# Performance work log

Hardware: AMD Instinct MI355X
Metric: run time of the kernel (lower is better)

The kernel has to match this reference:

```python
import jax, jax.numpy as jnp
import numpy as np

N_NODES = 100000
N_EDGES = 1600000
D_FEAT = 64
K = 5


def setup_inputs() -> dict:
    key = jax.random.key(0)
    k1, k2, k3 = jax.random.split(key, 3)
    feat = jax.random.normal(k1, (N_NODES, D_FEAT), dtype=jnp.float32)
    theta = jnp.asarray([1.0, -0.8, 0.45, -0.2, 0.08], dtype=jnp.float32)
    src = jax.random.randint(k2, (N_EDGES,), 0, N_NODES, dtype=jnp.int32)
    dst = jax.random.randint(k3, (N_EDGES,), 0, N_NODES, dtype=jnp.int32)
    return {"feat": feat, "theta": theta, "src": src, "dst": dst}


def reference(feat, theta, src, dst):
    n = feat.shape[0]
    # in-degrees: number of edges terminating at each node, clamped to >= 1
    deg = jax.ops.segment_sum(jnp.ones_like(dst, dtype=feat.dtype), dst, num_segments=n)
    d_invsqrt = jnp.maximum(deg, 1.0) ** -0.5  # [N]
    d_invsqrt = d_invsqrt[:, None]  # [N, 1]

    def unn_laplacian(x):
        scaled = x * d_invsqrt  # [N, D]
        agg = jax.ops.segment_sum(scaled[src], dst, num_segments=n)  # [N, D]
        return x - agg * d_invsqrt

    h = theta[0] * feat
    for k in range(1, theta.shape[0]):
        feat = unn_laplacian(feat)
        h = h + theta[k] * feat
    return h
```

## Files before the change

### kernel.cpp

```cpp
#include <hip/hip_runtime.h>
#include <hip/hip_bf16.h>
#include <hip/hip_fp16.h>

#define WG 256
#define WGB 1024
#define D 64
#define MAXNB 1024

__device__ inline float ld_mixed(const void* p, int bf, long i) {
    if (bf) {
        unsigned short u = ((const unsigned short*)p)[i];
        return __uint_as_float(((unsigned int)u) << 16);
    }
    return ((const float*)p)[i];
}

__global__ void k_detect(const void* __restrict__ theta, int* __restrict__ flag) {
    unsigned int w = *(const unsigned int*)theta;
    *flag = (w == 0x3F800000u) ? 0 : 1;
}


__global__ __launch_bounds__(WGB) void kc_hist(
        const int* __restrict__ dst, int E, int NBc, int CPB,
        int* __restrict__ histmat) {
    __shared__ int h[MAXNB];
    int B = blockIdx.x, t = threadIdx.x;
    for (int i = t; i < NBc; i += WGB) h[i] = 0;
    __syncthreads();
    int base = B * CPB;
    int end = min(base + CPB, E);
    for (int e = base + t; e < end; e += WGB)
        atomicAdd(&h[dst[e] >> 8], 1);
    __syncthreads();
    for (int i = t; i < NBc; i += WGB)
        histmat[(long)i * NBc + B] = h[i];
}

__global__ void k_scan1(const int* __restrict__ in, int M,
                        int* __restrict__ out, int* __restrict__ part) {
    __shared__ int s[WG];
    int g = blockIdx.x * WG + threadIdx.x;
    int t = threadIdx.x;
    s[t] = (g < M) ? in[g] : 0;
    __syncthreads();
    for (int o = 1; o < WG; o <<= 1) {
        int v = (t >= o) ? s[t - o] : 0;
        __syncthreads();
        s[t] += v;
        __syncthreads();
    }
    if (g < M) out[g + 1] = s[t];
    if (t == WG - 1) part[blockIdx.x] = s[t];
}

__global__ void k_scan2(int* __restrict__ part, int P) {
    __shared__ int s[1024];
    int t = threadIdx.x;
    s[t] = (t < P) ? part[t] : 0;
    __syncthreads();
    for (int o = 1; o < 1024; o <<= 1) {
        int v = (t >= o) ? s[t - o] : 0;
        __syncthreads();
        s[t] += v;
        __syncthreads();
    }
    if (t < P) part[t] = (t == 0) ? 0 : s[t - 1];
}

__global__ void k_scan3(int* __restrict__ out, int M, const int* __restrict__ part) {
    int g = blockIdx.x * WG + threadIdx.x;
    if (g < M) out[g + 1] += part[blockIdx.x];
    if (g == 0) out[0] = 0;
}

__global__ __launch_bounds__(WGB) void kc_scatter(
        const int* __restrict__ src, const int* __restrict__ dst, int E,
        int NBc, int CPB, const int* __restrict__ scanned,
        int2* __restrict__ tmp) {
    __shared__ int off[MAXNB];
    int B = blockIdx.x, t = threadIdx.x;
    for (int i = t; i < NBc; i += WGB)
        off[i] = scanned[(long)i * NBc + B];
    __syncthreads();
    int base = B * CPB;
    int end = min(base + CPB, E);
    for (int e = base + t; e < end; e += WGB) {
        int d = dst[e];
        int pos = atomicAdd(&off[d >> 8], 1);
        int2 p; p.x = src[e]; p.y = d;
        tmp[pos] = p;
    }
}

__global__ __launch_bounds__(WGB) void kf(
        const int2* __restrict__ tmp, const int* __restrict__ scanned,
        int NBc, int N, int E, int* __restrict__ ptr,
        float* __restrict__ dinv, float* __restrict__ dsqrt,
        int* __restrict__ csr) {
    __shared__ int h[256];
    __shared__ int pfx[256];
    __shared__ int cnt[256];
    int B = blockIdx.x, t = threadIdx.x;
    int rbase = scanned[(long)B * NBc];
    int rend  = scanned[(long)(B + 1) * NBc];
    if (t < 256) h[t] = 0;
    __syncthreads();
    for (int e = rbase + t; e < rend; e += WGB)
        atomicAdd(&h[tmp[e].y & 255], 1);
    __syncthreads();
    if (t < 256) pfx[t] = h[t];
    __syncthreads();
    for (int o = 1; o < 256; o <<= 1) {
        int v = 0;
        if (t < 256 && t >= o) v = pfx[t - o];
        __syncthreads();
        if (t < 256) pfx[t] += v;
        __syncthreads();
    }
    if (t < 256) {
        int ex = pfx[t] - h[t];
        int node = B * 256 + t;
        if (node < N) {
            ptr[node] = rbase + ex;
            float d = (float)h[t];
            d = d < 1.f ? 1.f : d;
            dinv[node]  = rsqrtf(d);
            dsqrt[node] = sqrtf(d);
        }
        cnt[t] = rbase + ex;
    }
    if (B == 0 && t == 0) ptr[N] = E;
    __syncthreads();
    for (int e = rbase + t; e < rend; e += WGB) {
        int2 p = tmp[e];
        int pos = atomicAdd(&cnt[p.y & 255], 1);
        csr[pos] = p.x;
    }
}


__global__ void k_init(const void* __restrict__ feat, const void* __restrict__ theta,
                       const int* __restrict__ flag, const float* __restrict__ dinv,
                       long NF, __half* __restrict__ xs, __half* __restrict__ h) {
    int bf = *flag;
    long g = (long)blockIdx.x * WG + threadIdx.x;
    if (g < NF) {
        float f = ld_mixed(feat, bf, g);
        float th0 = ld_mixed(theta, bf, 0);
        float w = dinv[g >> 6];
        xs[g] = __float2half_rn(f * w);
        h[g]  = __float2half_rn(th0 * f);
    }
}

__global__ __launch_bounds__(WG) void k_spmv(
        const __half* __restrict__ xs,
        const float* __restrict__ dinv, const float* __restrict__ dsqrt,
        const int* __restrict__ ptr, const int* __restrict__ csr,
        const void* __restrict__ theta, const int* __restrict__ flag, int k,
        int N, __half* __restrict__ xsn, __half* __restrict__ h,
        void* __restrict__ out, int last) {
    int wv = (int)(((unsigned)blockIdx.x * blockDim.x + threadIdx.x) >> 6);
    int lane = threadIdx.x & 63;
    int node = 2 * wv + (lane >> 5);
    int l = lane & 31;
    bool valid = node < N;
    int nc = valid ? node : 0;
    int s0 = ptr[nc];
    int s1 = valid ? ptr[nc + 1] : s0;

    const __half2* xs2 = (const __half2*)xs;
    float ax = 0.f, ay = 0.f;
    int e = s0;
    for (; e + 8 <= s1; e += 8) {
        int idx[8];
#pragma unroll
        for (int j = 0; j < 8; ++j) idx[j] = csr[e + j];
        __half2 a[8];
#pragma unroll
        for (int j = 0; j < 8; ++j) a[j] = xs2[idx[j] * 32 + l];
#pragma unroll
        for (int j = 0; j < 8; ++j) {
            float2 f = __half22float2(a[j]);
            ax += f.x; ay += f.y;
        }
    }
    if (e + 4 <= s1) {
        int idx[4];
#pragma unroll
        for (int j = 0; j < 4; ++j) idx[j] = csr[e + j];
        __half2 a[4];
#pragma unroll
        for (int j = 0; j < 4; ++j) a[j] = xs2[idx[j] * 32 + l];
#pragma unroll
        for (int j = 0; j < 4; ++j) {
            float2 f = __half22float2(a[j]);
            ax += f.x; ay += f.y;
        }
        e += 4;
    }
    for (; e < s1; ++e) {
        float2 f = __half22float2(xs2[csr[e] * 32 + l]);
        ax += f.x; ay += f.y;
    }

    if (!valid) return;
    long o = (long)node * 32 + l;
    float w = dinv[node];
    float ds = dsqrt[node];
    float2 xsv = __half22float2(xs2[o]);
    float vx = xsv.x * ds - w * ax;
    float vy = xsv.y * ds - w * ay;
    int bf = *flag;
    float th = ld_mixed(theta, bf, k);
    float2 hv = __half22float2(((const __half2*)h)[o]);
    hv.x += th * vx;
    hv.y += th * vy;
    if (last) {
        if (bf) {
            __hip_bfloat162 r;
            r.x = __float2bfloat16(hv.x);
            r.y = __float2bfloat16(hv.y);
            ((__hip_bfloat162*)out)[o] = r;
        } else {
            float2 r; r.x = hv.x; r.y = hv.y;
            ((float2*)out)[o] = r;
        }
    } else {
        ((__half2*)xsn)[o] = __floats2half2_rn(vx * w, vy * w);
        ((__half2*)h)[o]   = __floats2half2_rn(hv.x, hv.y);
    }
}

extern "C" void kernel_launch(void* const* d_in, const int* in_sizes, int n_in,
                              void* d_out, int out_size, void* d_ws, size_t ws_size,
                              hipStream_t stream) {
    const void* feat  = d_in[0];
    const void* theta = d_in[1];
    const int*  src   = (const int*)d_in[2];
    const int*  dst   = (const int*)d_in[3];
    long NF = in_sizes[0];
    int  N  = (int)(NF / D);
    int  E  = in_sizes[2];

    int NBc = (N + 255) >> 8;
    int CPB = (E + NBc - 1) / NBc;
    int M   = NBc * NBc;

    char* w = (char*)d_ws;
    size_t off = 0;
    auto alloc = [&](size_t b) -> void* {
        void* p = w + off;
        off = (off + b + 255) & ~(size_t)255;
        return p;
    };
    int*    histmat = (int*)alloc((size_t)M * 4);
    int*    scanned = (int*)alloc(((size_t)M + 1) * 4);
    int*    part    = (int*)alloc(1024 * 4);
    int2*   tmp     = (int2*)alloc((size_t)E * 8);
    int*    ptr     = (int*)alloc(((size_t)N + 1) * 4);
    int*    csr     = (int*)alloc((size_t)E * 4);
    float*  dinv    = (float*)alloc((size_t)N * 4);
    float*  dsqrt   = (float*)alloc((size_t)N * 4);
    int*    flag    = (int*)alloc(4);
    __half* xs_a    = (__half*)alloc((size_t)NF * 2);
    __half* xs_b    = (__half*)alloc((size_t)NF * 2);
    __half* h       = (__half*)alloc((size_t)NF * 2);

    int sbl = (M + WG - 1) / WG;
    int fbl = (int)((NF + WG - 1) / WG);
    int wbl = ((N + 1) / 2 + 3) / 4;

    k_detect<<<1, 1, 0, stream>>>(theta, flag);
    kc_hist<<<NBc, WGB, 0, stream>>>(dst, E, NBc, CPB, histmat);
    k_scan1<<<sbl, WG, 0, stream>>>(histmat, M, scanned, part);
    k_scan2<<<1, 1024, 0, stream>>>(part, sbl);
    k_scan3<<<sbl, WG, 0, stream>>>(scanned, M, part);
    kc_scatter<<<NBc, WGB, 0, stream>>>(src, dst, E, NBc, CPB, scanned, tmp);
    kf<<<NBc, WGB, 0, stream>>>(tmp, scanned, NBc, N, E, ptr, dinv, dsqrt, csr);
    k_init<<<fbl, WG, 0, stream>>>(feat, theta, flag, dinv, NF, xs_a, h);

    __half* xa = xs_a;
    __half* xb = xs_b;
    for (int k = 1; k <= 4; ++k) {
        int last = (k == 4);
        k_spmv<<<wbl, WG, 0, stream>>>(xa, dinv, dsqrt, ptr, csr, theta, flag, k,
                                       N, xb, h, d_out, last);
        __half* t = xa; xa = xb; xb = t;
    }
}
```

Measured before the change: 297.0 us.

## Fold detect and scan stages into neighbors, pack CSR temp, add nontemporal accesses

Removes the detect, scan2 and scan3 launches by moving flag detection into the histogram kernel and recomputing the block-partial scan redundantly inside the scatter and finalize kernels. The temporary edge buffer is packed from int2 to a single 32-bit word, with src in the low 24 bits and the local dst in the high 8 bits, halving its traffic. Nontemporal loads and stores are added for csr indices and the h/xs streams in init and spmv. The 24-bit src packing assumes fewer than 16M nodes, and every scatter/finalize block now does a redundant 1024-wide scan.

```diff
diff --git a/kernel.cpp b/kernel.cpp
--- a/kernel.cpp
+++ b/kernel.cpp
@@ -15,17 +15,17 @@
     return ((const float*)p)[i];
 }
 
-__global__ void k_detect(const void* __restrict__ theta, int* __restrict__ flag) {
-    unsigned int w = *(const unsigned int*)theta;
-    *flag = (w == 0x3F800000u) ? 0 : 1;
-}
-
 
 __global__ __launch_bounds__(WGB) void kc_hist(
         const int* __restrict__ dst, int E, int NBc, int CPB,
-        int* __restrict__ histmat) {
+        int* __restrict__ histmat,
+        const void* __restrict__ theta, int* __restrict__ flag) {
     __shared__ int h[MAXNB];
     int B = blockIdx.x, t = threadIdx.x;
+    if (B == 0 && t == 0) {
+        unsigned int w = *(const unsigned int*)theta;
+        *flag = (w == 0x3F800000u) ? 0 : 1;
+    }
     for (int i = t; i < NBc; i += WGB) h[i] = 0;
     __syncthreads();
     int base = B * CPB;
@@ -42,7 +42,8 @@
     __shared__ int s[WG];
     int g = blockIdx.x * WG + threadIdx.x;
     int t = threadIdx.x;
-    s[t] = (g < M) ? in[g] : 0;
+    int v0 = (g < M) ? in[g] : 0;
+    s[t] = v0;
     __syncthreads();
     for (int o = 1; o < WG; o <<= 1) {
         int v = (t >= o) ? s[t - o] : 0;
@@ -50,64 +51,79 @@
         s[t] += v;
         __syncthreads();
     }
-    if (g < M) out[g + 1] = s[t];
+    if (g < M) out[g] = s[t] - v0;
     if (t == WG - 1) part[blockIdx.x] = s[t];
-}
-
-__global__ void k_scan2(int* __restrict__ part, int P) {
-    __shared__ int s[1024];
-    int t = threadIdx.x;
-    s[t] = (t < P) ? part[t] : 0;
-    __syncthreads();
-    for (int o = 1; o < 1024; o <<= 1) {
-        int v = (t >= o) ? s[t - o] : 0;
-        __syncthreads();
-        s[t] += v;
-        __syncthreads();
-    }
-    if (t < P) part[t] = (t == 0) ? 0 : s[t - 1];
-}
-
-__global__ void k_scan3(int* __restrict__ out, int M, const int* __restrict__ part) {
-    int g = blockIdx.x * WG + threadIdx.x;
-    if (g < M) out[g + 1] += part[blockIdx.x];
-    if (g == 0) out[0] = 0;
 }
 
 __global__ __launch_bounds__(WGB) void kc_scatter(
         const int* __restrict__ src, const int* __restrict__ dst, int E,
-        int NBc, int CPB, const int* __restrict__ scanned,
-        int2* __restrict__ tmp) {
+        int NBc, int CPB, const int* __restrict__ outx,
+        const int* __restrict__ part, int P,
+        unsigned int* __restrict__ tmp) {
     __shared__ int off[MAXNB];
+    __shared__ int ps[1024];
+    __shared__ int pex[1024];
     int B = blockIdx.x, t = threadIdx.x;
-    for (int i = t; i < NBc; i += WGB)
-        off[i] = scanned[(long)i * NBc + B];
+    int pv = (t < P) ? part[t] : 0;
+    ps[t] = pv;
+    __syncthreads();
+    for (int o = 1; o < 1024; o <<= 1) {
+        int v = (t >= o) ? ps[t - o] : 0;
+        __syncthreads();
+        ps[t] += v;
+        __syncthreads();
+    }
+    pex[t] = ps[t] - pv;
+    __syncthreads();
+    for (int i = t; i < NBc; i += WGB) {
+        long g = (long)i * NBc + B;
+        off[i] = outx[g] + pex[g >> 8];
+    }
     __syncthreads();
     int base = B * CPB;
     int end = min(base + CPB, E);
     for (int e = base + t; e < end; e += WGB) {
         int d = dst[e];
         int pos = atomicAdd(&off[d >> 8], 1);
-        int2 p; p.x = src[e]; p.y = d;
-        tmp[pos] = p;
+        tmp[pos] = (unsigned)src[e] | ((unsigned)(d & 255) << 24);
     }
 }
 
 __global__ __launch_bounds__(WGB) void kf(
-        const int2* __restrict__ tmp, const int* __restrict__ scanned,
+        const unsigned int* __restrict__ tmp, const int* __restrict__ outx,
+        const int* __restrict__ part, int P,
         int NBc, int N, int E, int* __restrict__ ptr,
         float* __restrict__ dinv, float* __restrict__ dsqrt,
         int* __restrict__ csr) {
     __shared__ int h[256];
     __shared__ int pfx[256];
     __shared__ int cnt[256];
+    __shared__ int ps[1024];
+    __shared__ int pex[1024];
     int B = blockIdx.x, t = threadIdx.x;
-    int rbase = scanned[(long)B * NBc];
-    int rend  = scanned[(long)(B + 1) * NBc];
+    int pv = (t < P) ? part[t] : 0;
+    ps[t] = pv;
+    __syncthreads();
+    for (int o = 1; o < 1024; o <<= 1) {
+        int v = (t >= o) ? ps[t - o] : 0;
+        __syncthreads();
+        ps[t] += v;
+        __syncthreads();
+    }
+    pex[t] = ps[t] - pv;
+    __syncthreads();
+    long g1 = (long)B * NBc;
+    int rbase = outx[g1] + pex[g1 >> 8];
+    int rend;
+    if (B == NBc - 1) rend = E;
+    else {
+        long g2 = (long)(B + 1) * NBc;
+        rend = outx[g2] + pex[g2 >> 8];
+    }
     if (t < 256) h[t] = 0;
     __syncthreads();
     for (int e = rbase + t; e < rend; e += WGB)
-        atomicAdd(&h[tmp[e].y & 255], 1);
+        atomicAdd(&h[tmp[e] >> 24], 1);
     __syncthreads();
     if (t < 256) pfx[t] = h[t];
     __syncthreads();
@@ -133,9 +149,9 @@
     if (B == 0 && t == 0) ptr[N] = E;
     __syncthreads();
     for (int e = rbase + t; e < rend; e += WGB) {
-        int2 p = tmp[e];
-        int pos = atomicAdd(&cnt[p.y & 255], 1);
-        csr[pos] = p.x;
+        unsigned p = tmp[e];
+        int pos = atomicAdd(&cnt[p >> 24], 1);
+        csr[pos] = (int)(p & 0xFFFFFF);
     }
 }
 
@@ -150,7 +166,9 @@
         float th0 = ld_mixed(theta, bf, 0);
         float w = dinv[g >> 6];
         xs[g] = __float2half_rn(f * w);
-        h[g]  = __float2half_rn(th0 * f);
+        __half hv = __float2half_rn(th0 * f);
+        unsigned short hr = *(unsigned short*)&hv;
+        __builtin_nontemporal_store(hr, (unsigned short*)h + g);
     }
 }
 
@@ -176,7 +194,7 @@
     for (; e + 8 <= s1; e += 8) {
         int idx[8];
 #pragma unroll
-        for (int j = 0; j < 8; ++j) idx[j] = csr[e + j];
+        for (int j = 0; j < 8; ++j) idx[j] = __builtin_nontemporal_load(&csr[e + j]);
         __half2 a[8];
 #pragma unroll
         for (int j = 0; j < 8; ++j) a[j] = xs2[idx[j] * 32 + l];
@@ -189,7 +207,7 @@
     if (e + 4 <= s1) {
         int idx[4];
 #pragma unroll
-        for (int j = 0; j < 4; ++j) idx[j] = csr[e + j];
+        for (int j = 0; j < 4; ++j) idx[j] = __builtin_nontemporal_load(&csr[e + j]);
         __half2 a[4];
 #pragma unroll
         for (int j = 0; j < 4; ++j) a[j] = xs2[idx[j] * 32 + l];
@@ -214,7 +232,8 @@
     float vy = xsv.y * ds - w * ay;
     int bf = *flag;
     float th = ld_mixed(theta, bf, k);
-    float2 hv = __half22float2(((const __half2*)h)[o]);
+    unsigned hraw = __builtin_nontemporal_load((const unsigned int*)h + o);
+    float2 hv = __half22float2(*(__half2*)&hraw);
     hv.x += th * vx;
     hv.y += th * vy;
     if (last) {
@@ -228,8 +247,10 @@
             ((float2*)out)[o] = r;
         }
     } else {
-        ((__half2*)xsn)[o] = __floats2half2_rn(vx * w, vy * w);
-        ((__half2*)h)[o]   = __floats2half2_rn(hv.x, hv.y);
+        __half2 xw = __floats2half2_rn(vx * w, vy * w);
+        __builtin_nontemporal_store(*(unsigned*)&xw, (unsigned int*)xsn + o);
+        __half2 hw = __floats2half2_rn(hv.x, hv.y);
+        __builtin_nontemporal_store(*(unsigned*)&hw, (unsigned int*)h + o);
     }
 }
 
@@ -247,6 +268,7 @@
     int NBc = (N + 255) >> 8;
     int CPB = (E + NBc - 1) / NBc;
     int M   = NBc * NBc;
+    int sbl = (M + WG - 1) / WG;
 
     char* w = (char*)d_ws;
     size_t off = 0;
@@ -255,30 +277,26 @@
         off = (off + b + 255) & ~(size_t)255;
         return p;
     };
-    int*    histmat = (int*)alloc((size_t)M * 4);
-    int*    scanned = (int*)alloc(((size_t)M + 1) * 4);
-    int*    part    = (int*)alloc(1024 * 4);
-    int2*   tmp     = (int2*)alloc((size_t)E * 8);
-    int*    ptr     = (int*)alloc(((size_t)N + 1) * 4);
-    int*    csr     = (int*)alloc((size_t)E * 4);
-    float*  dinv    = (float*)alloc((size_t)N * 4);
-    float*  dsqrt   = (float*)alloc((size_t)N * 4);
-    int*    flag    = (int*)alloc(4);
-    __half* xs_a    = (__half*)alloc((size_t)NF * 2);
-    __half* xs_b    = (__half*)alloc((size_t)NF * 2);
-    __half* h       = (__half*)alloc((size_t)NF * 2);
-
-    int sbl = (M + WG - 1) / WG;
+    int*      histmat = (int*)alloc((size_t)M * 4);
+    int*      outx    = (int*)alloc((size_t)M * 4);
+    int*      part    = (int*)alloc(1024 * 4);
+    unsigned* tmp     = (unsigned*)alloc((size_t)E * 4);
+    int*      ptr     = (int*)alloc(((size_t)N + 1) * 4);
+    int*      csr     = (int*)alloc((size_t)E * 4);
+    float*    dinv    = (float*)alloc((size_t)N * 4);
+    float*    dsqrt   = (float*)alloc((size_t)N * 4);
+    int*      flag    = (int*)alloc(4);
+    __half*   xs_a    = (__half*)alloc((size_t)NF * 2);
+    __half*   xs_b    = (__half*)alloc((size_t)NF * 2);
+    __half*   h       = (__half*)alloc((size_t)NF * 2);
+
     int fbl = (int)((NF + WG - 1) / WG);
     int wbl = ((N + 1) / 2 + 3) / 4;
 
-    k_detect<<<1, 1, 0, stream>>>(theta, flag);
-    kc_hist<<<NBc, WGB, 0, stream>>>(dst, E, NBc, CPB, histmat);
-    k_scan1<<<sbl, WG, 0, stream>>>(histmat, M, scanned, part);
-    k_scan2<<<1, 1024, 0, stream>>>(part, sbl);
-    k_scan3<<<sbl, WG, 0, stream>>>(scanned, M, part);
-    kc_scatter<<<NBc, WGB, 0, stream>>>(src, dst, E, NBc, CPB, scanned, tmp);
-    kf<<<NBc, WGB, 0, stream>>>(tmp, scanned, NBc, N, E, ptr, dinv, dsqrt, csr);
+    kc_hist<<<NBc, WGB, 0, stream>>>(dst, E, NBc, CPB, histmat, theta, flag);
+    k_scan1<<<sbl, WG, 0, stream>>>(histmat, M, outx, part);
+    kc_scatter<<<NBc, WGB, 0, stream>>>(src, dst, E, NBc, CPB, outx, part, sbl, tmp);
+    kf<<<NBc, WGB, 0, stream>>>(tmp, outx, part, sbl, NBc, N, E, ptr, dinv, dsqrt, csr);
     k_init<<<fbl, WG, 0, stream>>>(feat, theta, flag, dinv, NF, xs_a, h);
 
     __half* xa = xs_a;
```

After: 329.0 us. 1.11x slower.
